# Performance work log

Hardware: AMD Instinct MI355X
Metric: run time of the kernel (lower is better)

Reference implementation:

```python
import jax, jax.numpy as jnp
import numpy as np
from jax import lax

STRIDE = 1
PAD = 1  # module pads 1 on each side whenever padding != 0


def setup_inputs() -> dict:
    key = jax.random.key(0)
    kx, kw, kb = jax.random.split(key, 3)
    x = jax.random.normal(kx, (4096, 4096), dtype=jnp.float32)
    weight = jax.random.normal(kw, (15, 15), dtype=jnp.float32)
    bias = jax.random.normal(kb, (1,), dtype=jnp.float32)
    return {"x": x, "weight": weight, "bias": bias}


def reference(x, weight, bias):
    # Single-channel 2D cross-correlation with constant zero padding of 1 and
    # stride STRIDE, plus a scalar bias. lax.conv_general_dilated computes
    # correlation (no kernel flip), matching the torch corr2d loop exactly.
    out = lax.conv_general_dilated(
        x[None, None, :, :],          # NCHW, N=C=1
        weight[None, None, :, :],      # OIHW, O=I=1
        window_strides=(STRIDE, STRIDE),
        padding=[(PAD, PAD), (PAD, PAD)],
        dimension_numbers=("NCHW", "OIHW", "NCHW"),
    )[0, 0]
    return out + bias[0]
```

## Files before the change

kernel.cpp:

```cpp
#include <hip/hip_runtime.h>

#define IN_N   4096
#define OW     4084
#define KS     15
#define TILE   64
#define XROWS  78
#define XCOLS  80
#define XS     88
#define NBX    64
#define NBY    64

typedef __attribute__((ext_vector_type(8))) short v8s;
typedef __attribute__((ext_vector_type(4))) float v4f;

__device__ __forceinline__ unsigned short f2bf(float f) {
    union { float f; unsigned u; } c; c.f = f;
    unsigned r = c.u + 0x7fff + ((c.u >> 16) & 1);
    return (unsigned short)(r >> 16);
}

__global__ void build_B(const float* __restrict__ w, unsigned short* __restrict__ Bg) {
    int ky = blockIdx.x;
    int e  = threadIdx.x;
    int n = e & 15, quad = e >> 4;
    unsigned short vals[8];
    #pragma unroll
    for (int j = 0; j < 8; ++j) {
        int d = quad * 8 + j - n;
        vals[j] = (d >= 0 && d < KS) ? f2bf(w[ky * KS + d]) : (unsigned short)0;
    }
    *(v8s*)(&Bg[(ky * 64 + e) * 8]) = *(const v8s*)vals;
}

__global__ __launch_bounds__(256, 6) void conv2d_mfma2(
    const float* __restrict__ x, const unsigned short* __restrict__ Bg,
    const float* __restrict__ bias, float* __restrict__ out)
{
    __shared__ unsigned short xtile[XROWS * XS] __attribute__((aligned(16)));

    const int tid = threadIdx.x;
    const int bx = blockIdx.x, by = blockIdx.y;
    const int X0 = bx * TILE;
    const int Y0 = by * TILE;

    const int tx = tid % 40;
    const int ty = tid / 40;
    const bool interior = (bx > 0) & (bx < NBX - 1) & (by > 0) & (by < NBY - 1);

    if (ty < 6) {
        unsigned short* dst = &xtile[ty * XS + 2 * tx];
        if (interior) {
            const float* xr = x + (size_t)(Y0 - 1 + ty) * IN_N + (X0 - 1 + 2 * tx);
            #pragma unroll
            for (int i = 0; i < 13; ++i) {
                float f0 = xr[0], f1 = xr[1];
                *(unsigned*)dst = (unsigned)f2bf(f0) | ((unsigned)f2bf(f1) << 16);
                xr  += 6 * IN_N;
                dst += 6 * XS;
            }
        } else {
            const int gc0 = X0 - 1 + 2 * tx;
            #pragma unroll
            for (int i = 0; i < 13; ++i) {
                int gr = Y0 - 1 + ty + 6 * i;
                float f0 = 0.0f, f1 = 0.0f;
                if ((unsigned)gr < (unsigned)IN_N) {
                    const float* xr = x + (size_t)gr * IN_N;
                    if ((unsigned)gc0       < (unsigned)IN_N) f0 = xr[gc0];
                    if ((unsigned)(gc0 + 1) < (unsigned)IN_N) f1 = xr[gc0 + 1];
                }
                *(unsigned*)dst = (unsigned)f2bf(f0) | ((unsigned)f2bf(f1) << 16);
                dst += 6 * XS;
            }
        }
    }
    __syncthreads();

    const int lane = tid & 63;
    const int wv   = tid >> 6;
    const int m    = lane & 15;
    const int quad = lane >> 4;

    v4f acc[4];
    #pragma unroll
    for (int t = 0; t < 4; ++t) acc[t] = (v4f){0.f, 0.f, 0.f, 0.f};

    const v8s* Bgv = (const v8s*)Bg;
    v8s bcur = Bgv[lane];
    const unsigned short* arow = &xtile[(wv * 16 + m) * XS + quad * 8];

    #pragma unroll
    for (int ky = 0; ky < KS; ++ky) {
        v8s bnext = (ky < KS - 1) ? Bgv[(ky + 1) * 64 + lane] : bcur;
        v8s a0 = *(const v8s*)(arow + 0);
        v8s a1 = *(const v8s*)(arow + 16);
        v8s a2 = *(const v8s*)(arow + 32);
        v8s a3 = *(const v8s*)(arow + 48);
        acc[0] = __builtin_amdgcn_mfma_f32_16x16x32_bf16(a0, bcur, acc[0], 0, 0, 0);
        acc[1] = __builtin_amdgcn_mfma_f32_16x16x32_bf16(a1, bcur, acc[1], 0, 0, 0);
        acc[2] = __builtin_amdgcn_mfma_f32_16x16x32_bf16(a2, bcur, acc[2], 0, 0, 0);
        acc[3] = __builtin_amdgcn_mfma_f32_16x16x32_bf16(a3, bcur, acc[3], 0, 0, 0);
        arow += XS;
        bcur = bnext;
    }

    const float bv = bias[0];
    const int orow0 = Y0 + wv * 16 + quad * 4;
    const int ocol0 = X0 + m;
    if (interior | ((bx < NBX - 1) & (by < NBY - 1))) {
        float* o0 = &out[(size_t)orow0 * OW + ocol0];
        #pragma unroll
        for (int t = 0; t < 4; ++t) {
            #pragma unroll
            for (int r = 0; r < 4; ++r)
                o0[(size_t)r * OW + t * 16] = acc[t][r] + bv;
        }
    } else {
        #pragma unroll
        for (int t = 0; t < 4; ++t) {
            int oc = ocol0 + t * 16;
            if (oc < OW) {
                #pragma unroll
                for (int r = 0; r < 4; ++r) {
                    int orow = orow0 + r;
                    if (orow < OW)
                        out[(size_t)orow * OW + oc] = acc[t][r] + bv;
                }
            }
        }
    }
}

extern "C" void kernel_launch(void* const* d_in, const int* in_sizes, int n_in,
                              void* d_out, int out_size, void* d_ws, size_t ws_size,
                              hipStream_t stream) {
    const float* x    = (const float*)d_in[0];
    const float* w    = (const float*)d_in[1];
    const float* bias = (const float*)d_in[2];
    float* out        = (float*)d_out;
    unsigned short* Bg = (unsigned short*)d_ws;

    build_B<<<dim3(KS), dim3(64), 0, stream>>>(w, Bg);
    dim3 grid(NBX, NBY);
    conv2d_mfma2<<<grid, dim3(256), 0, stream>>>(x, Bg, bias, out);
}
```

Before: 138.9 us.

## Switch to fp16 MFMA with packed conversion and wider aligned tile loads

Converts inputs to fp16 with the hardware packed round-toward-zero convert instead of manual bf16 rounding, and uses the f16 MFMA. The staging load shifts the tile start by one column (weights shifted to match) so each thread can do aligned 8-byte float2 loads of four values per row. Occupancy hint is raised from 6 to 8 blocks. fp16 narrows the dynamic range and rounds toward zero, which could affect accuracy on large values.

```diff
diff --git a/kernel.cpp b/kernel.cpp
--- a/kernel.cpp
+++ b/kernel.cpp
@@ -5,19 +5,16 @@
 #define KS     15
 #define TILE   64
 #define XROWS  78
-#define XCOLS  80
 #define XS     88
 #define NBX    64
 #define NBY    64
 
-typedef __attribute__((ext_vector_type(8))) short v8s;
-typedef __attribute__((ext_vector_type(4))) float v4f;
-
-__device__ __forceinline__ unsigned short f2bf(float f) {
-    union { float f; unsigned u; } c; c.f = f;
-    unsigned r = c.u + 0x7fff + ((c.u >> 16) & 1);
-    return (unsigned short)(r >> 16);
-}
+typedef __attribute__((ext_vector_type(8))) short     v8s;
+typedef __attribute__((ext_vector_type(8))) _Float16  v8h;
+typedef __attribute__((ext_vector_type(2))) _Float16  v2h;
+typedef __attribute__((ext_vector_type(4))) float     v4f;
+typedef __attribute__((ext_vector_type(2))) float     v2f;
+typedef __attribute__((ext_vector_type(2))) unsigned  v2u;
 
 __global__ void build_B(const float* __restrict__ w, unsigned short* __restrict__ Bg) {
     int ky = blockIdx.x;
@@ -26,13 +23,16 @@
     unsigned short vals[8];
     #pragma unroll
     for (int j = 0; j < 8; ++j) {
-        int d = quad * 8 + j - n;
-        vals[j] = (d >= 0 && d < KS) ? f2bf(w[ky * KS + d]) : (unsigned short)0;
+        int d = quad * 8 + j - 1 - n;
+        _Float16 h = (_Float16)0.0f;
+        if (d >= 0 && d < KS) h = (_Float16)w[ky * KS + d];
+        union { _Float16 hh; unsigned short u; } cv; cv.hh = h;
+        vals[j] = cv.u;
     }
     *(v8s*)(&Bg[(ky * 64 + e) * 8]) = *(const v8s*)vals;
 }
 
-__global__ __launch_bounds__(256, 6) void conv2d_mfma2(
+__global__ __launch_bounds__(256, 8) void conv2d_mfma3(
     const float* __restrict__ x, const unsigned short* __restrict__ Bg,
     const float* __restrict__ bias, float* __restrict__ out)
 {
@@ -42,35 +42,48 @@
     const int bx = blockIdx.x, by = blockIdx.y;
     const int X0 = bx * TILE;
     const int Y0 = by * TILE;
-
-    const int tx = tid % 40;
-    const int ty = tid / 40;
     const bool interior = (bx > 0) & (bx < NBX - 1) & (by > 0) & (by < NBY - 1);
 
-    if (ty < 6) {
-        unsigned short* dst = &xtile[ty * XS + 2 * tx];
+    if (tid < 240) {
+        const int tcol = tid % 20;
+        const int trow = tid / 20;
+        const int c0 = 4 * tcol;
+        unsigned short* dst = &xtile[trow * XS + c0];
         if (interior) {
-            const float* xr = x + (size_t)(Y0 - 1 + ty) * IN_N + (X0 - 1 + 2 * tx);
+            const float* xr = x + (size_t)(Y0 - 1 + trow) * IN_N + (X0 - 2 + c0);
             #pragma unroll
-            for (int i = 0; i < 13; ++i) {
-                float f0 = xr[0], f1 = xr[1];
-                *(unsigned*)dst = (unsigned)f2bf(f0) | ((unsigned)f2bf(f1) << 16);
-                xr  += 6 * IN_N;
-                dst += 6 * XS;
+            for (int i = 0; i < 7; ++i) {
+                if (i < 6 || trow < 6) {
+                    v2f f01 = *(const v2f*)xr;
+                    v2f f23 = *(const v2f*)(xr + 2);
+                    v2u p;
+                    p.x = __builtin_bit_cast(unsigned, __builtin_amdgcn_cvt_pkrtz(f01.x, f01.y));
+                    p.y = __builtin_bit_cast(unsigned, __builtin_amdgcn_cvt_pkrtz(f23.x, f23.y));
+                    *(v2u*)dst = p;
+                }
+                xr  += 12 * (size_t)IN_N;
+                dst += 12 * XS;
             }
         } else {
-            const int gc0 = X0 - 1 + 2 * tx;
+            const int gc0 = X0 - 2 + c0;
             #pragma unroll
-            for (int i = 0; i < 13; ++i) {
-                int gr = Y0 - 1 + ty + 6 * i;
-                float f0 = 0.0f, f1 = 0.0f;
-                if ((unsigned)gr < (unsigned)IN_N) {
-                    const float* xr = x + (size_t)gr * IN_N;
-                    if ((unsigned)gc0       < (unsigned)IN_N) f0 = xr[gc0];
-                    if ((unsigned)(gc0 + 1) < (unsigned)IN_N) f1 = xr[gc0 + 1];
+            for (int i = 0; i < 7; ++i) {
+                int row = trow + 12 * i;
+                if (row < XROWS) {
+                    int gr = Y0 - 1 + row;
+                    float f0 = 0.f, f1 = 0.f, f2 = 0.f, f3 = 0.f;
+                    if ((unsigned)gr < (unsigned)IN_N) {
+                        const float* xr = x + (size_t)gr * IN_N;
+                        if ((unsigned)(gc0 + 0) < (unsigned)IN_N) f0 = xr[gc0 + 0];
+                        if ((unsigned)(gc0 + 1) < (unsigned)IN_N) f1 = xr[gc0 + 1];
+                        if ((unsigned)(gc0 + 2) < (unsigned)IN_N) f2 = xr[gc0 + 2];
+                        if ((unsigned)(gc0 + 3) < (unsigned)IN_N) f3 = xr[gc0 + 3];
+                    }
+                    v2u p;
+                    p.x = __builtin_bit_cast(unsigned, __builtin_amdgcn_cvt_pkrtz(f0, f1));
+                    p.y = __builtin_bit_cast(unsigned, __builtin_amdgcn_cvt_pkrtz(f2, f3));
+                    *(v2u*)(&xtile[row * XS + c0]) = p;
                 }
-                *(unsigned*)dst = (unsigned)f2bf(f0) | ((unsigned)f2bf(f1) << 16);
-                dst += 6 * XS;
             }
         }
     }
@@ -85,21 +98,21 @@
     #pragma unroll
     for (int t = 0; t < 4; ++t) acc[t] = (v4f){0.f, 0.f, 0.f, 0.f};
 
-    const v8s* Bgv = (const v8s*)Bg;
-    v8s bcur = Bgv[lane];
+    const v8h* Bgv = (const v8h*)Bg;
+    v8h bcur = Bgv[lane];
     const unsigned short* arow = &xtile[(wv * 16 + m) * XS + quad * 8];
 
     #pragma unroll
     for (int ky = 0; ky < KS; ++ky) {
-        v8s bnext = (ky < KS - 1) ? Bgv[(ky + 1) * 64 + lane] : bcur;
-        v8s a0 = *(const v8s*)(arow + 0);
-        v8s a1 = *(const v8s*)(arow + 16);
-        v8s a2 = *(const v8s*)(arow + 32);
-        v8s a3 = *(const v8s*)(arow + 48);
-        acc[0] = __builtin_amdgcn_mfma_f32_16x16x32_bf16(a0, bcur, acc[0], 0, 0, 0);
-        acc[1] = __builtin_amdgcn_mfma_f32_16x16x32_bf16(a1, bcur, acc[1], 0, 0, 0);
-        acc[2] = __builtin_amdgcn_mfma_f32_16x16x32_bf16(a2, bcur, acc[2], 0, 0, 0);
-        acc[3] = __builtin_amdgcn_mfma_f32_16x16x32_bf16(a3, bcur, acc[3], 0, 0, 0);
+        v8h bnext = (ky < KS - 1) ? Bgv[(ky + 1) * 64 + lane] : bcur;
+        v8h a0 = *(const v8h*)(arow + 0);
+        v8h a1 = *(const v8h*)(arow + 16);
+        v8h a2 = *(const v8h*)(arow + 32);
+        v8h a3 = *(const v8h*)(arow + 48);
+        acc[0] = __builtin_amdgcn_mfma_f32_16x16x32_f16(a0, bcur, acc[0], 0, 0, 0);
+        acc[1] = __builtin_amdgcn_mfma_f32_16x16x32_f16(a1, bcur, acc[1], 0, 0, 0);
+        acc[2] = __builtin_amdgcn_mfma_f32_16x16x32_f16(a2, bcur, acc[2], 0, 0, 0);
+        acc[3] = __builtin_amdgcn_mfma_f32_16x16x32_f16(a3, bcur, acc[3], 0, 0, 0);
         arow += XS;
         bcur = bnext;
     }
@@ -142,5 +155,5 @@
 
     build_B<<<dim3(KS), dim3(64), 0, stream>>>(w, Bg);
     dim3 grid(NBX, NBY);
-    conv2d_mfma2<<<grid, dim3(256), 0, stream>>>(x, Bg, bias, out);
+    conv2d_mfma3<<<grid, dim3(256), 0, stream>>>(x, Bg, bias, out);
 }
```

New measurement: 141.0 us. No clear change (+1.5%).
